# Kernel optimization log

Hardware: AMD Instinct MI355X
Metric: run time of the kernel (lower is better)

Reference implementation:

```python
import jax, jax.numpy as jnp
import numpy as np

N, IN_DIM, OUT_DIM = 8192, 256, 64
NEG_INF = -9e15
SLOPE = 0.2


def setup_inputs() -> dict:
    key = jax.random.key(0)
    k1, k2, k3, k4 = jax.random.split(key, 4)
    h = jax.random.normal(k1, (N, IN_DIM), dtype=jnp.float32)
    adj = jax.random.randint(k2, (N, N), 0, 2, dtype=jnp.int32)
    W = jax.random.normal(k3, (IN_DIM, OUT_DIM), dtype=jnp.float32) * (1.0 / np.sqrt(IN_DIM))
    a = jax.random.normal(k4, (2 * OUT_DIM,), dtype=jnp.float32) * (1.0 / np.sqrt(2 * OUT_DIM))
    return {"h": h, "adj": adj, "W": W, "a": a}


def reference(h, adj, W, a):
    # Wh: [N, F]
    Wh = h @ W
    F = Wh.shape[-1]
    # a([Wh_i ; Wh_j]) decomposes: score_ij = a_left.Wh_i + a_right.Wh_j
    f_i = Wh @ a[:F]          # [N]
    f_j = Wh @ a[F:]          # [N]
    e = f_i[:, None] + f_j[None, :]            # [N, N] broadcast sum
    e = jnp.where(e >= 0, e, SLOPE * e)         # leaky relu (0.2)
    e = jnp.where(adj > 0, e, jnp.float32(NEG_INF))
    alpha = jax.nn.softmax(e, axis=1)           # row softmax over neighbors j
    return alpha @ Wh                            # [N, F]
```

## Files before the change

### kernel.cpp

```cpp
#include <hip/hip_runtime.h>
#include <hip/hip_fp16.h>

#define NN 8192
#define KDIM 256
#define FDIM 64
#define CBLK 1024
#define NSEG (NN / CBLK)

typedef __attribute__((ext_vector_type(8))) _Float16 f16x8;
typedef __attribute__((ext_vector_type(4))) float f32x4;
typedef __attribute__((ext_vector_type(4))) int i32x4;

union H2U { __half2 h; unsigned u; };
union HU  { __half h; unsigned short u; };

__device__ __forceinline__ unsigned h2u(__half2 h) { H2U x; x.h = h; return x.u; }

__device__ __forceinline__ unsigned pkmul(unsigned a, unsigned b) {
    unsigned d; asm("v_pk_mul_f16 %0, %1, %2" : "=v"(d) : "v"(a), "v"(b)); return d;
}
__device__ __forceinline__ unsigned pkmax(unsigned a, unsigned b) {
    unsigned d; asm("v_pk_max_f16 %0, %1, %2" : "=v"(d) : "v"(a), "v"(b)); return d;
}

__device__ __forceinline__ float wred64(float v) {
    v += __shfl_xor(v, 1);
    v += __shfl_xor(v, 2);
    v += __shfl_xor(v, 4);
    v += __shfl_xor(v, 8);
    v += __shfl_xor(v, 16);
    v += __shfl_xor(v, 32);
    return v;
}

__global__ __launch_bounds__(256) void gat_phase1(
    const float* __restrict__ h, const float* __restrict__ W,
    const float* __restrict__ a, unsigned short* __restrict__ wfrag,
    float* __restrict__ fi, float* __restrict__ fj)
{
    __shared__ unsigned short wht_s[FDIM][20];
    const int tid = threadIdx.x;
    const int f  = tid & 63;
    const int rg = tid >> 6;
    const int i0 = blockIdx.x << 4;

    const float* __restrict__ h0 = h + (size_t)(i0 + rg * 4) * KDIM;
    const float* __restrict__ h1 = h0 + KDIM;
    const float* __restrict__ h2 = h0 + 2 * KDIM;
    const float* __restrict__ h3 = h0 + 3 * KDIM;

    float acc0 = 0.f, acc1 = 0.f, acc2 = 0.f, acc3 = 0.f;
    #pragma unroll 4
    for (int k4 = 0; k4 < KDIM / 4; ++k4) {
        const float4 r0 = *(const float4*)(h0 + k4 * 4);
        const float4 r1 = *(const float4*)(h1 + k4 * 4);
        const float4 r2 = *(const float4*)(h2 + k4 * 4);
        const float4 r3 = *(const float4*)(h3 + k4 * 4);
        const float w0 = W[(k4 * 4 + 0) * FDIM + f];
        const float w1 = W[(k4 * 4 + 1) * FDIM + f];
        const float w2 = W[(k4 * 4 + 2) * FDIM + f];
        const float w3 = W[(k4 * 4 + 3) * FDIM + f];
        acc0 += r0.x * w0 + r0.y * w1 + r0.z * w2 + r0.w * w3;
        acc1 += r1.x * w0 + r1.y * w1 + r1.z * w2 + r1.w * w3;
        acc2 += r2.x * w0 + r2.y * w1 + r2.z * w2 + r2.w * w3;
        acc3 += r3.x * w0 + r3.y * w1 + r3.z * w2 + r3.w * w3;
    }

    HU c0; c0.h = __float2half(acc0);
    HU c1; c1.h = __float2half(acc1);
    HU c2; c2.h = __float2half(acc2);
    HU c3; c3.h = __float2half(acc3);
    const int r0i = rg * 4;
    wht_s[f][r0i + 0] = c0.u;
    wht_s[f][r0i + 1] = c1.u;
    wht_s[f][r0i + 2] = c2.u;
    wht_s[f][r0i + 3] = c3.u;

    const float aL = a[f];
    const float aR = a[FDIM + f];
    float s;
    s = wred64(acc0 * aL); if (f == 0) fi[i0 + r0i + 0] = s;
    s = wred64(acc1 * aL); if (f == 0) fi[i0 + r0i + 1] = s;
    s = wred64(acc2 * aL); if (f == 0) fi[i0 + r0i + 2] = s;
    s = wred64(acc3 * aL); if (f == 0) fi[i0 + r0i + 3] = s;
    s = wred64(acc0 * aR); if (f == 0) fj[i0 + r0i + 0] = s;
    s = wred64(acc1 * aR); if (f == 0) fj[i0 + r0i + 1] = s;
    s = wred64(acc2 * aR); if (f == 0) fj[i0 + r0i + 2] = s;
    s = wred64(acc3 * aR); if (f == 0) fj[i0 + r0i + 3] = s;

    __syncthreads();
    if (tid < 128) {
        const int li2 = tid & 15;
        const int q2  = (tid >> 4) & 1;
        const int b   = tid >> 5;
        const int t   = i0 >> 5;
        const int hh  = (i0 >> 4) & 1;
        const int feat = b * 16 + li2;
        const ushort4 lo = *(const ushort4*)&wht_s[feat][q2 * 8];
        const ushort4 hi = *(const ushort4*)&wht_s[feat][q2 * 8 + 4];
        const int lg = (hh * 2 + q2) * 16 + li2;
        unsigned short* dst = wfrag + (size_t)t * 2048 + b * 512 + lg * 8;
        *(ushort4*)(dst)     = lo;
        *(ushort4*)(dst + 4) = hi;
    }
}

__global__ __launch_bounds__(256, 4) void gat_fused(
    const int* __restrict__ adj, const unsigned short* __restrict__ wfrag,
    const float* __restrict__ fi, const float* __restrict__ fjg,
    float* __restrict__ vpart, float* __restrict__ zpart)
{
    __shared__ unsigned mask_lds[16][33];
    __shared__ unsigned Ebuf[1024];
    __shared__ float red[2 * 16 * 64];
    __shared__ float zred[4][16];

    const int tid = threadIdx.x;
    const int w  = tid >> 6;
    const int l  = tid & 63;
    const int li = l & 15;
    const int q  = l >> 4;
    const int qo = q * 8;
    const int bid = blockIdx.x;
    const int seg = bid & (NSEG - 1);
    const int i0  = (bid / NSEG) << 4;

    unsigned* E1p = Ebuf;
    unsigned* E2p = Ebuf + 512;
    for (int t = tid; t < 512; t += 256) {
        const float2 f2 = ((const float2*)fjg)[seg * 512 + t];
        E1p[t] = h2u(__floats2half2_rn(__expf(f2.x), __expf(f2.y)));
        E2p[t] = h2u(__floats2half2_rn(__expf(0.2f * f2.x), __expf(0.2f * f2.y)));
    }

    const int wsel = (l & 7) * 4;
    #pragma unroll
    for (int rp = 0; rp < 2; ++rp) {
        const int r0 = 4 * w + 2 * rp;
        const i32x4* __restrict__ p0 =
            (const i32x4*)(adj + (size_t)(i0 + r0) * NN + seg * CBLK);
        const i32x4* __restrict__ p1 = p0 + (NN / 4);
        i32x4 v[8];
        #pragma unroll
        for (int k = 0; k < 4; ++k) v[k]     = p0[k * 64 + l];
        #pragma unroll
        for (int k = 0; k < 4; ++k) v[4 + k] = p1[k * 64 + l];
        #pragma unroll
        for (int k = 0; k < 8; ++k) {
            const i32x4 x = v[k];
            unsigned nib = (unsigned)(x[0] > 0) | ((unsigned)(x[1] > 0) << 1)
                         | ((unsigned)(x[2] > 0) << 2) | ((unsigned)(x[3] > 0) << 3);
            unsigned p = nib << wsel;
            p |= __shfl_xor(p, 1);
            p |= __shfl_xor(p, 2);
            p |= __shfl_xor(p, 4);
            const int rr = r0 + (k >> 2);
            if ((l & 7) == 0) mask_lds[rr][(k & 3) * 8 + (l >> 3)] = p;
        }
    }

    const float fiv = fi[i0 + li];
    const unsigned e1i2 = h2u(__floats2half2_rn(__expf(fiv), __expf(fiv)));
    const unsigned e2i2 = h2u(__floats2half2_rn(__expf(0.2f * fiv), __expf(0.2f * fiv)));
    const unsigned short* __restrict__ wf =
        wfrag + (size_t)(seg * 32) * 2048 + l * 8;

    __syncthreads();

    f32x4 acc0 = {0.f, 0.f, 0.f, 0.f};
    f32x4 acc1 = {0.f, 0.f, 0.f, 0.f};
    f32x4 acc2 = {0.f, 0.f, 0.f, 0.f};
    f32x4 acc3 = {0.f, 0.f, 0.f, 0.f};
    f32x4 accz = {0.f, 0.f, 0.f, 0.f};
    const f16x8 ones = { (_Float16)1.f, (_Float16)1.f, (_Float16)1.f, (_Float16)1.f,
                         (_Float16)1.f, (_Float16)1.f, (_Float16)1.f, (_Float16)1.f };

    #pragma unroll 4
    for (int s = 0; s < 8; ++s) {
        const int tw = w + 4 * s;
        const unsigned mword = mask_lds[li][tw];
        const unsigned mq8 = (mword >> qo) & 0xFFu;
        const int ep = tw * 16 + q * 4;
        const uint4 e1w = *(const uint4*)(E1p + ep);
        const uint4 e2w = *(const uint4*)(E2p + ep);
        const unsigned short* wt = wf + (size_t)tw * 2048;
        const f16x8 b0 = *(const f16x8*)(wt);
        const f16x8 b1 = *(const f16x8*)(wt + 512);
        const f16x8 b2 = *(const f16x8*)(wt + 1024);
        const f16x8 b3 = *(const f16x8*)(wt + 1536);

        const unsigned mm0 = ((mq8 &   1u) ? 0x0000FFFFu : 0u) | ((mq8 &   2u) ? 0xFFFF0000u : 0u);
        const unsigned mm1 = ((mq8 &   4u) ? 0x0000FFFFu : 0u) | ((mq8 &   8u) ? 0xFFFF0000u : 0u);
        const unsigned mm2 = ((mq8 &  16u) ? 0x0000FFFFu : 0u) | ((mq8 &  32u) ? 0xFFFF0000u : 0u);
        const unsigned mm3 = ((mq8 &  64u) ? 0x0000FFFFu : 0u) | ((mq8 & 128u) ? 0xFFFF0000u : 0u);

        union { unsigned u[4]; f16x8 v; } af;
        af.u[0] = pkmax(pkmul(e1i2, e1w.x), pkmul(e2i2, e2w.x)) & mm0;
        af.u[1] = pkmax(pkmul(e1i2, e1w.y), pkmul(e2i2, e2w.y)) & mm1;
        af.u[2] = pkmax(pkmul(e1i2, e1w.z), pkmul(e2i2, e2w.z)) & mm2;
        af.u[3] = pkmax(pkmul(e1i2, e1w.w), pkmul(e2i2, e2w.w)) & mm3;

        acc0 = __builtin_amdgcn_mfma_f32_16x16x32_f16(af.v, b0, acc0, 0, 0, 0);
        acc1 = __builtin_amdgcn_mfma_f32_16x16x32_f16(af.v, b1, acc1, 0, 0, 0);
        acc2 = __builtin_amdgcn_mfma_f32_16x16x32_f16(af.v, b2, acc2, 0, 0, 0);
        acc3 = __builtin_amdgcn_mfma_f32_16x16x32_f16(af.v, b3, acc3, 0, 0, 0);
        accz = __builtin_amdgcn_mfma_f32_16x16x32_f16(af.v, ones, accz, 0, 0, 0);
    }

    if (li == 0) {
        #pragma unroll
        for (int r = 0; r < 4; ++r)
            zred[w][q * 4 + r] = accz[r];
    }
    if (w < 2) {
        #pragma unroll
        for (int r = 0; r < 4; ++r) {
            red[(w * 16 + q * 4 + r) * 64 + 0 * 16 + li] = acc0[r];
            red[(w * 16 + q * 4 + r) * 64 + 1 * 16 + li] = acc1[r];
            red[(w * 16 + q * 4 + r) * 64 + 2 * 16 + li] = acc2[r];
            red[(w * 16 + q * 4 + r) * 64 + 3 * 16 + li] = acc3[r];
        }
    }
    __syncthreads();
    if (w >= 2) {
        #pragma unroll
        for (int r = 0; r < 4; ++r) {
            red[((w - 2) * 16 + q * 4 + r) * 64 + 0 * 16 + li] += acc0[r];
            red[((w - 2) * 16 + q * 4 + r) * 64 + 1 * 16 + li] += acc1[r];
            red[((w - 2) * 16 + q * 4 + r) * 64 + 2 * 16 + li] += acc2[r];
            red[((w - 2) * 16 + q * 4 + r) * 64 + 3 * 16 + li] += acc3[r];
        }
    }
    __syncthreads();

    const int f  = tid & 63;
    const int ig = tid >> 6;
    #pragma unroll
    for (int cc = 0; cc < 4; ++cc) {
        const int i = cc * 4 + ig;
        const float v = red[(0 * 16 + i) * 64 + f] + red[(1 * 16 + i) * 64 + f];
        vpart[(size_t)(seg * NN + i0 + i) * FDIM + f] = v;
        if (f == 0) {
            const float zz = (zred[0][i] + zred[1][i]) + (zred[2][i] + zred[3][i]);
            zpart[seg * NN + i0 + i] = zz;
        }
    }
}

__global__ __launch_bounds__(256) void gat_merge(
    const float* __restrict__ vpart, const float* __restrict__ zpart,
    float* __restrict__ out)
{
    const int g = blockIdx.x * 256 + threadIdx.x;
    const int row = g >> 4;
    float4 v = ((const float4*)vpart)[g];
    float z = zpart[row];
    #pragma unroll
    for (int k = 1; k < NSEG; ++k) {
        const float4 b = ((const float4*)vpart)[g + (size_t)k * NN * (FDIM / 4)];
        v.x += b.x; v.y += b.y; v.z += b.z; v.w += b.w;
        z += zpart[row + k * NN];
    }
    float4 o;
    o.x = v.x / z; o.y = v.y / z; o.z = v.z / z; o.w = v.w / z;
    ((float4*)out)[g] = o;
}

extern "C" void kernel_launch(void* const* d_in, const int* in_sizes, int n_in,
                              void* d_out, int out_size, void* d_ws, size_t ws_size,
                              hipStream_t stream) {
    const float* h   = (const float*)d_in[0];
    const int*   adj = (const int*)d_in[1];
    const float* W   = (const float*)d_in[2];
    const float* a   = (const float*)d_in[3];
    float* out = (float*)d_out;

    unsigned short* wfrag = (unsigned short*)d_ws;
    float* fi = (float*)((char*)d_ws + (size_t)NN * FDIM * 2);
    float* fj = fi + NN;
    float* vpart = (float*)((char*)d_ws + (2u << 20));
    float* zpart = (float*)((char*)d_ws + (18u << 20));

    gat_phase1<<<NN / 16, 256, 0, stream>>>(h, W, a, wfrag, fi, fj);
    gat_fused<<<(NN / 16) * NSEG, 256, 0, stream>>>(adj, wfrag, fi, fj, vpart, zpart);
    gat_merge<<<NN * FDIM / 1024, 256, 0, stream>>>(vpart, zpart, out);
}
```

Before: 92.20 us.

## Process 32 rows per block to reuse W fragments and E tiles across two row groups

Each fused block now handles 32 adjacency rows instead of 16, loading the adjacency mask for both groups. Each loaded W fragment and E1/E2 vector feeds two sets of MFMA accumulators, halving B-operand and exp-table traffic per row and halving the grid size. The block index mapping also changes so segment is the slow dimension, which changes which blocks share wfrag data in cache. The cost is more accumulator registers, more adjacency loads per block before the first sync, and a serialized two-pass LDS reduction at the end.

```diff
diff --git a/kernel.cpp b/kernel.cpp
--- a/kernel.cpp
+++ b/kernel.cpp
@@ -6,6 +6,7 @@
 #define FDIM 64
 #define CBLK 1024
 #define NSEG (NN / CBLK)
+#define RBLK 32
 
 typedef __attribute__((ext_vector_type(8))) _Float16 f16x8;
 typedef __attribute__((ext_vector_type(4))) float f32x4;
@@ -110,7 +111,7 @@
     const float* __restrict__ fi, const float* __restrict__ fjg,
     float* __restrict__ vpart, float* __restrict__ zpart)
 {
-    __shared__ unsigned mask_lds[16][33];
+    __shared__ unsigned mask_lds[RBLK][33];
     __shared__ unsigned Ebuf[1024];
     __shared__ float red[2 * 16 * 64];
     __shared__ float zred[4][16];
@@ -122,8 +123,8 @@
     const int q  = l >> 4;
     const int qo = q * 8;
     const int bid = blockIdx.x;
-    const int seg = bid & (NSEG - 1);
-    const int i0  = (bid / NSEG) << 4;
+    const int seg = bid >> 8;
+    const int i0  = (bid & 255) << 5;
 
     unsigned* E1p = Ebuf;
     unsigned* E2p = Ebuf + 512;
@@ -135,8 +136,8 @@
 
     const int wsel = (l & 7) * 4;
     #pragma unroll
-    for (int rp = 0; rp < 2; ++rp) {
-        const int r0 = 4 * w + 2 * rp;
+    for (int rp = 0; rp < 4; ++rp) {
+        const int r0 = 8 * w + 2 * rp;
         const i32x4* __restrict__ p0 =
             (const i32x4*)(adj + (size_t)(i0 + r0) * NN + seg * CBLK);
         const i32x4* __restrict__ p1 = p0 + (NN / 4);
@@ -159,27 +160,33 @@
         }
     }
 
-    const float fiv = fi[i0 + li];
-    const unsigned e1i2 = h2u(__floats2half2_rn(__expf(fiv), __expf(fiv)));
-    const unsigned e2i2 = h2u(__floats2half2_rn(__expf(0.2f * fiv), __expf(0.2f * fiv)));
+    const float fiv0 = fi[i0 + li];
+    const float fiv1 = fi[i0 + 16 + li];
+    const unsigned e1i2_0 = h2u(__floats2half2_rn(__expf(fiv0), __expf(fiv0)));
+    const unsigned e2i2_0 = h2u(__floats2half2_rn(__expf(0.2f * fiv0), __expf(0.2f * fiv0)));
+    const unsigned e1i2_1 = h2u(__floats2half2_rn(__expf(fiv1), __expf(fiv1)));
+    const unsigned e2i2_1 = h2u(__floats2half2_rn(__expf(0.2f * fiv1), __expf(0.2f * fiv1)));
     const unsigned short* __restrict__ wf =
         wfrag + (size_t)(seg * 32) * 2048 + l * 8;
 
     __syncthreads();
 
-    f32x4 acc0 = {0.f, 0.f, 0.f, 0.f};
-    f32x4 acc1 = {0.f, 0.f, 0.f, 0.f};
-    f32x4 acc2 = {0.f, 0.f, 0.f, 0.f};
-    f32x4 acc3 = {0.f, 0.f, 0.f, 0.f};
-    f32x4 accz = {0.f, 0.f, 0.f, 0.f};
+    f32x4 acc00 = {0.f, 0.f, 0.f, 0.f};
+    f32x4 acc01 = {0.f, 0.f, 0.f, 0.f};
+    f32x4 acc02 = {0.f, 0.f, 0.f, 0.f};
+    f32x4 acc03 = {0.f, 0.f, 0.f, 0.f};
+    f32x4 accz0 = {0.f, 0.f, 0.f, 0.f};
+    f32x4 acc10 = {0.f, 0.f, 0.f, 0.f};
+    f32x4 acc11 = {0.f, 0.f, 0.f, 0.f};
+    f32x4 acc12 = {0.f, 0.f, 0.f, 0.f};
+    f32x4 acc13 = {0.f, 0.f, 0.f, 0.f};
+    f32x4 accz1 = {0.f, 0.f, 0.f, 0.f};
     const f16x8 ones = { (_Float16)1.f, (_Float16)1.f, (_Float16)1.f, (_Float16)1.f,
                          (_Float16)1.f, (_Float16)1.f, (_Float16)1.f, (_Float16)1.f };
 
-    #pragma unroll 4
+    #pragma unroll 2
     for (int s = 0; s < 8; ++s) {
         const int tw = w + 4 * s;
-        const unsigned mword = mask_lds[li][tw];
-        const unsigned mq8 = (mword >> qo) & 0xFFu;
         const int ep = tw * 16 + q * 4;
         const uint4 e1w = *(const uint4*)(E1p + ep);
         const uint4 e2w = *(const uint4*)(E2p + ep);
@@ -189,60 +196,119 @@
         const f16x8 b2 = *(const f16x8*)(wt + 1024);
         const f16x8 b3 = *(const f16x8*)(wt + 1536);
 
-        const unsigned mm0 = ((mq8 &   1u) ? 0x0000FFFFu : 0u) | ((mq8 &   2u) ? 0xFFFF0000u : 0u);
-        const unsigned mm1 = ((mq8 &   4u) ? 0x0000FFFFu : 0u) | ((mq8 &   8u) ? 0xFFFF0000u : 0u);
-        const unsigned mm2 = ((mq8 &  16u) ? 0x0000FFFFu : 0u) | ((mq8 &  32u) ? 0xFFFF0000u : 0u);
-        const unsigned mm3 = ((mq8 &  64u) ? 0x0000FFFFu : 0u) | ((mq8 & 128u) ? 0xFFFF0000u : 0u);
-
-        union { unsigned u[4]; f16x8 v; } af;
-        af.u[0] = pkmax(pkmul(e1i2, e1w.x), pkmul(e2i2, e2w.x)) & mm0;
-        af.u[1] = pkmax(pkmul(e1i2, e1w.y), pkmul(e2i2, e2w.y)) & mm1;
-        af.u[2] = pkmax(pkmul(e1i2, e1w.z), pkmul(e2i2, e2w.z)) & mm2;
-        af.u[3] = pkmax(pkmul(e1i2, e1w.w), pkmul(e2i2, e2w.w)) & mm3;
-
-        acc0 = __builtin_amdgcn_mfma_f32_16x16x32_f16(af.v, b0, acc0, 0, 0, 0);
-        acc1 = __builtin_amdgcn_mfma_f32_16x16x32_f16(af.v, b1, acc1, 0, 0, 0);
-        acc2 = __builtin_amdgcn_mfma_f32_16x16x32_f16(af.v, b2, acc2, 0, 0, 0);
-        acc3 = __builtin_amdgcn_mfma_f32_16x16x32_f16(af.v, b3, acc3, 0, 0, 0);
-        accz = __builtin_amdgcn_mfma_f32_16x16x32_f16(af.v, ones, accz, 0, 0, 0);
-    }
-
+        {
+            const unsigned mq8 = (mask_lds[li][tw] >> qo) & 0xFFu;
+            const unsigned mm0 = ((mq8 &   1u) ? 0x0000FFFFu : 0u) | ((mq8 &   2u) ? 0xFFFF0000u : 0u);
+            const unsigned mm1 = ((mq8 &   4u) ? 0x0000FFFFu : 0u) | ((mq8 &   8u) ? 0xFFFF0000u : 0u);
+            const unsigned mm2 = ((mq8 &  16u) ? 0x0000FFFFu : 0u) | ((mq8 &  32u) ? 0xFFFF0000u : 0u);
+            const unsigned mm3 = ((mq8 &  64u) ? 0x0000FFFFu : 0u) | ((mq8 & 128u) ? 0xFFFF0000u : 0u);
+            union { unsigned u[4]; f16x8 v; } af;
+            af.u[0] = pkmax(pkmul(e1i2_0, e1w.x), pkmul(e2i2_0, e2w.x)) & mm0;
+            af.u[1] = pkmax(pkmul(e1i2_0, e1w.y), pkmul(e2i2_0, e2w.y)) & mm1;
+            af.u[2] = pkmax(pkmul(e1i2_0, e1w.z), pkmul(e2i2_0, e2w.z)) & mm2;
+            af.u[3] = pkmax(pkmul(e1i2_0, e1w.w), pkmul(e2i2_0, e2w.w)) & mm3;
+            acc00 = __builtin_amdgcn_mfma_f32_16x16x32_f16(af.v, b0, acc00, 0, 0, 0);
+            acc01 = __builtin_amdgcn_mfma_f32_16x16x32_f16(af.v, b1, acc01, 0, 0, 0);
+            acc02 = __builtin_amdgcn_mfma_f32_16x16x32_f16(af.v, b2, acc02, 0, 0, 0);
+            acc03 = __builtin_amdgcn_mfma_f32_16x16x32_f16(af.v, b3, acc03, 0, 0, 0);
+            accz0 = __builtin_amdgcn_mfma_f32_16x16x32_f16(af.v, ones, accz0, 0, 0, 0);
+        }
+        {
+            const unsigned mq8 = (mask_lds[16 + li][tw] >> qo) & 0xFFu;
+            const unsigned mm0 = ((mq8 &   1u) ? 0x0000FFFFu : 0u) | ((mq8 &   2u) ? 0xFFFF0000u : 0u);
+            const unsigned mm1 = ((mq8 &   4u) ? 0x0000FFFFu : 0u) | ((mq8 &   8u) ? 0xFFFF0000u : 0u);
+            const unsigned mm2 = ((mq8 &  16u) ? 0x0000FFFFu : 0u) | ((mq8 &  32u) ? 0xFFFF0000u : 0u);
+            const unsigned mm3 = ((mq8 &  64u) ? 0x0000FFFFu : 0u) | ((mq8 & 128u) ? 0xFFFF0000u : 0u);
+            union { unsigned u[4]; f16x8 v; } af;
+            af.u[0] = pkmax(pkmul(e1i2_1, e1w.x), pkmul(e2i2_1, e2w.x)) & mm0;
+            af.u[1] = pkmax(pkmul(e1i2_1, e1w.y), pkmul(e2i2_1, e2w.y)) & mm1;
+            af.u[2] = pkmax(pkmul(e1i2_1, e1w.z), pkmul(e2i2_1, e2w.z)) & mm2;
+            af.u[3] = pkmax(pkmul(e1i2_1, e1w.w), pkmul(e2i2_1, e2w.w)) & mm3;
+            acc10 = __builtin_amdgcn_mfma_f32_16x16x32_f16(af.v, b0, acc10, 0, 0, 0);
+            acc11 = __builtin_amdgcn_mfma_f32_16x16x32_f16(af.v, b1, acc11, 0, 0, 0);
+            acc12 = __builtin_amdgcn_mfma_f32_16x16x32_f16(af.v, b2, acc12, 0, 0, 0);
+            acc13 = __builtin_amdgcn_mfma_f32_16x16x32_f16(af.v, b3, acc13, 0, 0, 0);
+            accz1 = __builtin_amdgcn_mfma_f32_16x16x32_f16(af.v, ones, accz1, 0, 0, 0);
+        }
+    }
+
+    __syncthreads();
     if (li == 0) {
         #pragma unroll
-        for (int r = 0; r < 4; ++r)
-            zred[w][q * 4 + r] = accz[r];
+        for (int r = 0; r < 4; ++r) zred[w][q * 4 + r] = accz0[r];
     }
     if (w < 2) {
         #pragma unroll
         for (int r = 0; r < 4; ++r) {
-            red[(w * 16 + q * 4 + r) * 64 + 0 * 16 + li] = acc0[r];
-            red[(w * 16 + q * 4 + r) * 64 + 1 * 16 + li] = acc1[r];
-            red[(w * 16 + q * 4 + r) * 64 + 2 * 16 + li] = acc2[r];
-            red[(w * 16 + q * 4 + r) * 64 + 3 * 16 + li] = acc3[r];
+            red[(w * 16 + q * 4 + r) * 64 + 0 * 16 + li] = acc00[r];
+            red[(w * 16 + q * 4 + r) * 64 + 1 * 16 + li] = acc01[r];
+            red[(w * 16 + q * 4 + r) * 64 + 2 * 16 + li] = acc02[r];
+            red[(w * 16 + q * 4 + r) * 64 + 3 * 16 + li] = acc03[r];
         }
     }
     __syncthreads();
     if (w >= 2) {
         #pragma unroll
         for (int r = 0; r < 4; ++r) {
-            red[((w - 2) * 16 + q * 4 + r) * 64 + 0 * 16 + li] += acc0[r];
-            red[((w - 2) * 16 + q * 4 + r) * 64 + 1 * 16 + li] += acc1[r];
-            red[((w - 2) * 16 + q * 4 + r) * 64 + 2 * 16 + li] += acc2[r];
-            red[((w - 2) * 16 + q * 4 + r) * 64 + 3 * 16 + li] += acc3[r];
-        }
-    }
-    __syncthreads();
-
-    const int f  = tid & 63;
-    const int ig = tid >> 6;
-    #pragma unroll
-    for (int cc = 0; cc < 4; ++cc) {
-        const int i = cc * 4 + ig;
-        const float v = red[(0 * 16 + i) * 64 + f] + red[(1 * 16 + i) * 64 + f];
-        vpart[(size_t)(seg * NN + i0 + i) * FDIM + f] = v;
-        if (f == 0) {
-            const float zz = (zred[0][i] + zred[1][i]) + (zred[2][i] + zred[3][i]);
-            zpart[seg * NN + i0 + i] = zz;
+            red[((w - 2) * 16 + q * 4 + r) * 64 + 0 * 16 + li] += acc00[r];
+            red[((w - 2) * 16 + q * 4 + r) * 64 + 1 * 16 + li] += acc01[r];
+            red[((w - 2) * 16 + q * 4 + r) * 64 + 2 * 16 + li] += acc02[r];
+            red[((w - 2) * 16 + q * 4 + r) * 64 + 3 * 16 + li] += acc03[r];
+        }
+    }
+    __syncthreads();
+    {
+        const int f  = tid & 63;
+        const int ig = tid >> 6;
+        #pragma unroll
+        for (int cc = 0; cc < 4; ++cc) {
+            const int i = cc * 4 + ig;
+            const float v = red[(0 * 16 + i) * 64 + f] + red[(1 * 16 + i) * 64 + f];
+            vpart[(size_t)(seg * NN + i0 + i) * FDIM + f] = v;
+            if (f == 0) {
+                const float zz = (zred[0][i] + zred[1][i]) + (zred[2][i] + zred[3][i]);
+                zpart[seg * NN + i0 + i] = zz;
+            }
+        }
+    }
+
+    __syncthreads();
+    if (li == 0) {
+        #pragma unroll
+        for (int r = 0; r < 4; ++r) zred[w][q * 4 + r] = accz1[r];
+    }
+    if (w < 2) {
+        #pragma unroll
+        for (int r = 0; r < 4; ++r) {
+            red[(w * 16 + q * 4 + r) * 64 + 0 * 16 + li] = acc10[r];
+            red[(w * 16 + q * 4 + r) * 64 + 1 * 16 + li] = acc11[r];
+            red[(w * 16 + q * 4 + r) * 64 + 2 * 16 + li] = acc12[r];
+            red[(w * 16 + q * 4 + r) * 64 + 3 * 16 + li] = acc13[r];
+        }
+    }
+    __syncthreads();
+    if (w >= 2) {
+        #pragma unroll
+        for (int r = 0; r < 4; ++r) {
+            red[((w - 2) * 16 + q * 4 + r) * 64 + 0 * 16 + li] += acc10[r];
+            red[((w - 2) * 16 + q * 4 + r) * 64 + 1 * 16 + li] += acc11[r];
+            red[((w - 2) * 16 + q * 4 + r) * 64 + 2 * 16 + li] += acc12[r];
+            red[((w - 2) * 16 + q * 4 + r) * 64 + 3 * 16 + li] += acc13[r];
+        }
+    }
+    __syncthreads();
+    {
+        const int f  = tid & 63;
+        const int ig = tid >> 6;
+        #pragma unroll
+        for (int cc = 0; cc < 4; ++cc) {
+            const int i = cc * 4 + ig;
+            const float v = red[(0 * 16 + i) * 64 + f] + red[(1 * 16 + i) * 64 + f];
+            vpart[(size_t)(seg * NN + i0 + 16 + i) * FDIM + f] = v;
+            if (f == 0) {
+                const float zz = (zred[0][i] + zred[1][i]) + (zred[2][i] + zred[3][i]);
+                zpart[seg * NN + i0 + 16 + i] = zz;
+            }
         }
     }
 }
@@ -282,6 +348,6 @@
     float* zpart = (float*)((char*)d_ws + (18u << 20));
 
     gat_phase1<<<NN / 16, 256, 0, stream>>>(h, W, a, wfrag, fi, fj);
-    gat_fused<<<(NN / 16) * NSEG, 256, 0, stream>>>(adj, wfrag, fi, fj, vpart, zpart);
+    gat_fused<<<(NN / RBLK) * NSEG, 256, 0, stream>>>(adj, wfrag, fi, fj, vpart, zpart);
     gat_merge<<<NN * FDIM / 1024, 256, 0, stream>>>(vpart, zpart, out);
 }
```

Measured after the change: 92.76 us. Within noise of the previous version (+0.6%).

## Stage Wh fragments in LDS and pipeline adj loads across row groups

Applied to the files above, without the earlier changes.

Halves the column segment to 512 and has each block loop over four 16-row groups, staging the segment's Wh fragments in shared memory once per block instead of reading them from global memory per row group. Adjacency loads for group g+2 and mask construction for g+1 are issued while group g's MFMA work runs, using a double-buffered mask, so memory latency can overlap compute. It doubles the number of partial segments, which enlarges the partial buffers and the merge traffic, and lowers the occupancy bound because the LDS footprint grows.

```diff
diff --git a/kernel.cpp b/kernel.cpp
--- a/kernel.cpp
+++ b/kernel.cpp
@@ -4,12 +4,15 @@
 #define NN 8192
 #define KDIM 256
 #define FDIM 64
-#define CBLK 1024
+#define CBLK 512
 #define NSEG (NN / CBLK)
+#define WPB  (CBLK / 32)
+#define ITER 4
 
 typedef __attribute__((ext_vector_type(8))) _Float16 f16x8;
 typedef __attribute__((ext_vector_type(4))) float f32x4;
 typedef __attribute__((ext_vector_type(4))) int i32x4;
+typedef __attribute__((ext_vector_type(4))) unsigned u32x4;
 
 union H2U { __half2 h; unsigned u; };
 union HU  { __half h; unsigned short u; };
@@ -105,13 +108,14 @@
     }
 }
 
-__global__ __launch_bounds__(256, 4) void gat_fused(
+__global__ __launch_bounds__(256, 2) void gat_fused(
     const int* __restrict__ adj, const unsigned short* __restrict__ wfrag,
     const float* __restrict__ fi, const float* __restrict__ fjg,
     float* __restrict__ vpart, float* __restrict__ zpart)
 {
-    __shared__ unsigned mask_lds[16][33];
-    __shared__ unsigned Ebuf[1024];
+    __shared__ unsigned short wfl[WPB * 2048];
+    __shared__ unsigned Ebuf[512];
+    __shared__ unsigned mask_lds[2][16][17];
     __shared__ float red[2 * 16 * 64];
     __shared__ float zred[4][16];
 
@@ -122,129 +126,148 @@
     const int q  = l >> 4;
     const int qo = q * 8;
     const int bid = blockIdx.x;
-    const int seg = bid & (NSEG - 1);
-    const int i0  = (bid / NSEG) << 4;
-
-    unsigned* E1p = Ebuf;
-    unsigned* E2p = Ebuf + 512;
-    for (int t = tid; t < 512; t += 256) {
-        const float2 f2 = ((const float2*)fjg)[seg * 512 + t];
-        E1p[t] = h2u(__floats2half2_rn(__expf(f2.x), __expf(f2.y)));
-        E2p[t] = h2u(__floats2half2_rn(__expf(0.2f * f2.x), __expf(0.2f * f2.y)));
+    const int seg = bid >> 7;
+    const int rb  = bid & 127;
+
+    {
+        const u32x4* src = (const u32x4*)(wfrag + (size_t)seg * WPB * 2048);
+        u32x4* dst = (u32x4*)wfl;
+        for (int t = tid; t < WPB * 2048 / 8; t += 256)
+            dst[t] = src[t];
+        const float2 f2 = ((const float2*)fjg)[seg * 256 + tid];
+        Ebuf[tid]       = h2u(__floats2half2_rn(__expf(f2.x), __expf(f2.y)));
+        Ebuf[256 + tid] = h2u(__floats2half2_rn(__expf(0.2f * f2.x), __expf(0.2f * f2.y)));
     }
 
     const int wsel = (l & 7) * 4;
-    #pragma unroll
-    for (int rp = 0; rp < 2; ++rp) {
-        const int r0 = 4 * w + 2 * rp;
-        const i32x4* __restrict__ p0 =
-            (const i32x4*)(adj + (size_t)(i0 + r0) * NN + seg * CBLK);
-        const i32x4* __restrict__ p1 = p0 + (NN / 4);
-        i32x4 v[8];
-        #pragma unroll
-        for (int k = 0; k < 4; ++k) v[k]     = p0[k * 64 + l];
-        #pragma unroll
-        for (int k = 0; k < 4; ++k) v[4 + k] = p1[k * 64 + l];
-        #pragma unroll
-        for (int k = 0; k < 8; ++k) {
-            const i32x4 x = v[k];
-            unsigned nib = (unsigned)(x[0] > 0) | ((unsigned)(x[1] > 0) << 1)
-                         | ((unsigned)(x[2] > 0) << 2) | ((unsigned)(x[3] > 0) << 3);
-            unsigned p = nib << wsel;
-            p |= __shfl_xor(p, 1);
-            p |= __shfl_xor(p, 2);
-            p |= __shfl_xor(p, 4);
-            const int rr = r0 + (k >> 2);
-            if ((l & 7) == 0) mask_lds[rr][(k & 3) * 8 + (l >> 3)] = p;
-        }
-    }
-
-    const float fiv = fi[i0 + li];
-    const unsigned e1i2 = h2u(__floats2half2_rn(__expf(fiv), __expf(fiv)));
-    const unsigned e2i2 = h2u(__floats2half2_rn(__expf(0.2f * fiv), __expf(0.2f * fiv)));
-    const unsigned short* __restrict__ wf =
-        wfrag + (size_t)(seg * 32) * 2048 + l * 8;
-
+    i32x4 v[8];
+
+    #define LOADADJ(g)                                                        \
+        do {                                                                  \
+            _Pragma("unroll")                                                 \
+            for (int r = 0; r < 4; ++r) {                                     \
+                const i32x4* rowp = (const i32x4*)(adj +                      \
+                    (size_t)(rb * 64 + (g) * 16 + 4 * w + r) * NN + seg * CBLK); \
+                v[r * 2 + 0] = rowp[l];                                       \
+                v[r * 2 + 1] = rowp[64 + l];                                  \
+            }                                                                 \
+        } while (0)
+
+    #define BALLOT(g)                                                         \
+        do {                                                                  \
+            _Pragma("unroll")                                                 \
+            for (int r = 0; r < 4; ++r)                                       \
+            for (int j = 0; j < 2; ++j) {                                     \
+                const i32x4 x = v[r * 2 + j];                                 \
+                unsigned nib = (unsigned)(x[0] > 0) | ((unsigned)(x[1] > 0) << 1) \
+                             | ((unsigned)(x[2] > 0) << 2) | ((unsigned)(x[3] > 0) << 3); \
+                unsigned p = nib << wsel;                                     \
+                p |= __shfl_xor(p, 1);                                        \
+                p |= __shfl_xor(p, 2);                                        \
+                p |= __shfl_xor(p, 4);                                        \
+                if ((l & 7) == 0)                                             \
+                    mask_lds[(g) & 1][4 * w + r][j * 8 + (l >> 3)] = p;       \
+            }                                                                 \
+        } while (0)
+
+    LOADADJ(0);
+    BALLOT(0);
+    LOADADJ(1);
     __syncthreads();
 
-    f32x4 acc0 = {0.f, 0.f, 0.f, 0.f};
-    f32x4 acc1 = {0.f, 0.f, 0.f, 0.f};
-    f32x4 acc2 = {0.f, 0.f, 0.f, 0.f};
-    f32x4 acc3 = {0.f, 0.f, 0.f, 0.f};
-    f32x4 accz = {0.f, 0.f, 0.f, 0.f};
+    const unsigned* E1p = Ebuf;
+    const unsigned* E2p = Ebuf + 256;
     const f16x8 ones = { (_Float16)1.f, (_Float16)1.f, (_Float16)1.f, (_Float16)1.f,
                          (_Float16)1.f, (_Float16)1.f, (_Float16)1.f, (_Float16)1.f };
 
-    #pragma unroll 4
-    for (int s = 0; s < 8; ++s) {
-        const int tw = w + 4 * s;
-        const unsigned mword = mask_lds[li][tw];
-        const unsigned mq8 = (mword >> qo) & 0xFFu;
-        const int ep = tw * 16 + q * 4;
-        const uint4 e1w = *(const uint4*)(E1p + ep);
-        const uint4 e2w = *(const uint4*)(E2p + ep);
-        const unsigned short* wt = wf + (size_t)tw * 2048;
-        const f16x8 b0 = *(const f16x8*)(wt);
-        const f16x8 b1 = *(const f16x8*)(wt + 512);
-        const f16x8 b2 = *(const f16x8*)(wt + 1024);
-        const f16x8 b3 = *(const f16x8*)(wt + 1536);
-
-        const unsigned mm0 = ((mq8 &   1u) ? 0x0000FFFFu : 0u) | ((mq8 &   2u) ? 0xFFFF0000u : 0u);
-        const unsigned mm1 = ((mq8 &   4u) ? 0x0000FFFFu : 0u) | ((mq8 &   8u) ? 0xFFFF0000u : 0u);
-        const unsigned mm2 = ((mq8 &  16u) ? 0x0000FFFFu : 0u) | ((mq8 &  32u) ? 0xFFFF0000u : 0u);
-        const unsigned mm3 = ((mq8 &  64u) ? 0x0000FFFFu : 0u) | ((mq8 & 128u) ? 0xFFFF0000u : 0u);
-
-        union { unsigned u[4]; f16x8 v; } af;
-        af.u[0] = pkmax(pkmul(e1i2, e1w.x), pkmul(e2i2, e2w.x)) & mm0;
-        af.u[1] = pkmax(pkmul(e1i2, e1w.y), pkmul(e2i2, e2w.y)) & mm1;
-        af.u[2] = pkmax(pkmul(e1i2, e1w.z), pkmul(e2i2, e2w.z)) & mm2;
-        af.u[3] = pkmax(pkmul(e1i2, e1w.w), pkmul(e2i2, e2w.w)) & mm3;
-
-        acc0 = __builtin_amdgcn_mfma_f32_16x16x32_f16(af.v, b0, acc0, 0, 0, 0);
-        acc1 = __builtin_amdgcn_mfma_f32_16x16x32_f16(af.v, b1, acc1, 0, 0, 0);
-        acc2 = __builtin_amdgcn_mfma_f32_16x16x32_f16(af.v, b2, acc2, 0, 0, 0);
-        acc3 = __builtin_amdgcn_mfma_f32_16x16x32_f16(af.v, b3, acc3, 0, 0, 0);
-        accz = __builtin_amdgcn_mfma_f32_16x16x32_f16(af.v, ones, accz, 0, 0, 0);
-    }
-
-    if (li == 0) {
+    for (int g = 0; g < ITER; ++g) {
+        const int i0 = rb * 64 + g * 16;
+        const float fiv = fi[i0 + li];
+        const unsigned e1i2 = h2u(__floats2half2_rn(__expf(fiv), __expf(fiv)));
+        const unsigned e2i2 = h2u(__floats2half2_rn(__expf(0.2f * fiv), __expf(0.2f * fiv)));
+
+        f32x4 acc0 = {0.f, 0.f, 0.f, 0.f};
+        f32x4 acc1 = {0.f, 0.f, 0.f, 0.f};
+        f32x4 acc2 = {0.f, 0.f, 0.f, 0.f};
+        f32x4 acc3 = {0.f, 0.f, 0.f, 0.f};
+        f32x4 accz = {0.f, 0.f, 0.f, 0.f};
+
         #pragma unroll
-        for (int r = 0; r < 4; ++r)
-            zred[w][q * 4 + r] = accz[r];
-    }
-    if (w < 2) {
-        #pragma unroll
-        for (int r = 0; r < 4; ++r) {
-            red[(w * 16 + q * 4 + r) * 64 + 0 * 16 + li] = acc0[r];
-            red[(w * 16 + q * 4 + r) * 64 + 1 * 16 + li] = acc1[r];
-            red[(w * 16 + q * 4 + r) * 64 + 2 * 16 + li] = acc2[r];
-            red[(w * 16 + q * 4 + r) * 64 + 3 * 16 + li] = acc3[r];
-        }
-    }
-    __syncthreads();
-    if (w >= 2) {
-        #pragma unroll
-        for (int r = 0; r < 4; ++r) {
-            red[((w - 2) * 16 + q * 4 + r) * 64 + 0 * 16 + li] += acc0[r];
-            red[((w - 2) * 16 + q * 4 + r) * 64 + 1 * 16 + li] += acc1[r];
-            red[((w - 2) * 16 + q * 4 + r) * 64 + 2 * 16 + li] += acc2[r];
-            red[((w - 2) * 16 + q * 4 + r) * 64 + 3 * 16 + li] += acc3[r];
-        }
-    }
-    __syncthreads();
-
-    const int f  = tid & 63;
-    const int ig = tid >> 6;
-    #pragma unroll
-    for (int cc = 0; cc < 4; ++cc) {
-        const int i = cc * 4 + ig;
-        const float v = red[(0 * 16 + i) * 64 + f] + red[(1 * 16 + i) * 64 + f];
-        vpart[(size_t)(seg * NN + i0 + i) * FDIM + f] = v;
-        if (f == 0) {
-            const float zz = (zred[0][i] + zred[1][i]) + (zred[2][i] + zred[3][i]);
-            zpart[seg * NN + i0 + i] = zz;
-        }
-    }
+        for (int s = 0; s < WPB / 4; ++s) {
+            const int tw = w + 4 * s;
+            const unsigned mq8 = (mask_lds[g & 1][li][tw] >> qo) & 0xFFu;
+            const int ep = tw * 16 + q * 4;
+            const uint4 e1w = *(const uint4*)(E1p + ep);
+            const uint4 e2w = *(const uint4*)(E2p + ep);
+            const unsigned short* wt = wfl + tw * 2048 + l * 8;
+            const f16x8 b0 = *(const f16x8*)(wt);
+            const f16x8 b1 = *(const f16x8*)(wt + 512);
+            const f16x8 b2 = *(const f16x8*)(wt + 1024);
+            const f16x8 b3 = *(const f16x8*)(wt + 1536);
+
+            const unsigned mm0 = ((mq8 &   1u) ? 0x0000FFFFu : 0u) | ((mq8 &   2u) ? 0xFFFF0000u : 0u);
+            const unsigned mm1 = ((mq8 &   4u) ? 0x0000FFFFu : 0u) | ((mq8 &   8u) ? 0xFFFF0000u : 0u);
+            const unsigned mm2 = ((mq8 &  16u) ? 0x0000FFFFu : 0u) | ((mq8 &  32u) ? 0xFFFF0000u : 0u);
+            const unsigned mm3 = ((mq8 &  64u) ? 0x0000FFFFu : 0u) | ((mq8 & 128u) ? 0xFFFF0000u : 0u);
+
+            union { unsigned u[4]; f16x8 vv; } af;
+            af.u[0] = pkmax(pkmul(e1i2, e1w.x), pkmul(e2i2, e2w.x)) & mm0;
+            af.u[1] = pkmax(pkmul(e1i2, e1w.y), pkmul(e2i2, e2w.y)) & mm1;
+            af.u[2] = pkmax(pkmul(e1i2, e1w.z), pkmul(e2i2, e2w.z)) & mm2;
+            af.u[3] = pkmax(pkmul(e1i2, e1w.w), pkmul(e2i2, e2w.w)) & mm3;
+
+            acc0 = __builtin_amdgcn_mfma_f32_16x16x32_f16(af.vv, b0, acc0, 0, 0, 0);
+            acc1 = __builtin_amdgcn_mfma_f32_16x16x32_f16(af.vv, b1, acc1, 0, 0, 0);
+            acc2 = __builtin_amdgcn_mfma_f32_16x16x32_f16(af.vv, b2, acc2, 0, 0, 0);
+            acc3 = __builtin_amdgcn_mfma_f32_16x16x32_f16(af.vv, b3, acc3, 0, 0, 0);
+            accz = __builtin_amdgcn_mfma_f32_16x16x32_f16(af.vv, ones, accz, 0, 0, 0);
+        }
+
+        if (g + 1 < ITER) BALLOT(g + 1);
+        if (g + 2 < ITER) LOADADJ(g + 2);
+
+        if (li == 0) {
+            #pragma unroll
+            for (int r = 0; r < 4; ++r) zred[w][q * 4 + r] = accz[r];
+        }
+        if (w < 2) {
+            #pragma unroll
+            for (int r = 0; r < 4; ++r) {
+                red[(w * 16 + q * 4 + r) * 64 + 0 * 16 + li] = acc0[r];
+                red[(w * 16 + q * 4 + r) * 64 + 1 * 16 + li] = acc1[r];
+                red[(w * 16 + q * 4 + r) * 64 + 2 * 16 + li] = acc2[r];
+                red[(w * 16 + q * 4 + r) * 64 + 3 * 16 + li] = acc3[r];
+            }
+        }
+        __syncthreads();
+        if (w >= 2) {
+            #pragma unroll
+            for (int r = 0; r < 4; ++r) {
+                red[((w - 2) * 16 + q * 4 + r) * 64 + 0 * 16 + li] += acc0[r];
+                red[((w - 2) * 16 + q * 4 + r) * 64 + 1 * 16 + li] += acc1[r];
+                red[((w - 2) * 16 + q * 4 + r) * 64 + 2 * 16 + li] += acc2[r];
+                red[((w - 2) * 16 + q * 4 + r) * 64 + 3 * 16 + li] += acc3[r];
+            }
+        }
+        __syncthreads();
+        {
+            const int f  = tid & 63;
+            const int ig = tid >> 6;
+            #pragma unroll
+            for (int cc = 0; cc < 4; ++cc) {
+                const int i = cc * 4 + ig;
+                const float vv = red[(0 * 16 + i) * 64 + f] + red[(1 * 16 + i) * 64 + f];
+                vpart[(size_t)(seg * NN + i0 + i) * FDIM + f] = vv;
+                if (f == 0) {
+                    const float zz = (zred[0][i] + zred[1][i]) + (zred[2][i] + zred[3][i]);
+                    zpart[seg * NN + i0 + i] = zz;
+                }
+            }
+        }
+        __syncthreads();
+    }
+    #undef LOADADJ
+    #undef BALLOT
 }
 
 __global__ __launch_bounds__(256) void gat_merge(
@@ -279,9 +302,9 @@
     float* fi = (float*)((char*)d_ws + (size_t)NN * FDIM * 2);
     float* fj = fi + NN;
     float* vpart = (float*)((char*)d_ws + (2u << 20));
-    float* zpart = (float*)((char*)d_ws + (18u << 20));
+    float* zpart = (float*)((char*)d_ws + (34u << 20));
 
     gat_phase1<<<NN / 16, 256, 0, stream>>>(h, W, a, wfrag, fi, fj);
-    gat_fused<<<(NN / 16) * NSEG, 256, 0, stream>>>(adj, wfrag, fi, fj, vpart, zpart);
+    gat_fused<<<NSEG * 128, 256, 0, stream>>>(adj, wfrag, fi, fj, vpart, zpart);
     gat_merge<<<NN * FDIM / 1024, 256, 0, stream>>>(vpart, zpart, out);
 }
```

After: 120.1 us. +30.3%, slower.
